# Performance work log

Hardware: AMD Instinct MI355X
Metric: run time of the kernel (lower is better)

Reference implementation:

```python
import jax, jax.numpy as jnp
import numpy as np

B, T, I, H, L = 256, 2000, 80, 20, 2
G = 4 * H  # gates i,f,g,o (PyTorch order)


def _lstm_dir(xg, w_hh, reverse):
    # xg: [B, T, 4H] precomputed input-gate contributions (incl. bias)
    # w_hh: [H, 4H]
    xg_t = jnp.swapaxes(xg, 0, 1)  # [T, B, 4H]
    if reverse:
        xg_t = xg_t[::-1]

    def step(carry, g_x):
        h, c = carry
        gates = g_x + h @ w_hh  # [B, 4H]
        i, f, g, o = jnp.split(gates, 4, axis=-1)
        c = jax.nn.sigmoid(f) * c + jax.nn.sigmoid(i) * jnp.tanh(g)
        h = jax.nn.sigmoid(o) * jnp.tanh(c)
        return (h, c), h

    h0 = jnp.zeros((xg.shape[0], H), xg.dtype)
    _, hs = jax.lax.scan(step, (h0, h0), xg_t)  # hs: [T, B, H]
    if reverse:
        hs = hs[::-1]
    return jnp.swapaxes(hs, 0, 1)  # [B, T, H]


def _bilstm_layer(x, w_ih, w_hh, b):
    # x: [B, T, in], w_ih: [2, in, 4H], w_hh: [2, H, 4H], b: [2, 4H]
    out = []
    for d in range(2):
        xg = jnp.einsum('bti,ig->btg', x, w_ih[d]) + b[d]
        out.append(_lstm_dir(xg, w_hh[d], reverse=(d == 1)))
    return jnp.concatenate(out, axis=-1)  # [B, T, 2H]


def setup_inputs() -> dict:
    key = jax.random.key(0)
    ks = jax.random.split(key, 9)
    s = 1.0 / np.sqrt(H)
    u = lambda k, shp: jax.random.uniform(k, shp, jnp.float32, -s, s)
    return {
        'x': jax.random.normal(ks[0], (B, T, I), jnp.float32),
        'w_ih_l0': u(ks[1], (2, I, G)),
        'w_hh_l0': u(ks[2], (2, H, G)),
        'b_l0': u(ks[3], (2, G)),
        'w_ih_l1': u(ks[4], (2, 2 * H, G)),
        'w_hh_l1': u(ks[5], (2, H, G)),
        'b_l1': u(ks[6], (2, G)),
        'fc_w': u(ks[7], (1, 2 * H)),
        'fc_b': u(ks[8], (1,)),
    }


def reference(x, w_ih_l0, w_hh_l0, b_l0, w_ih_l1, w_hh_l1, b_l1, fc_w, fc_b):
    h = _bilstm_layer(x, w_ih_l0, w_hh_l0, b_l0)      # [B, T, 2H]
    h = _bilstm_layer(h, w_ih_l1, w_hh_l1, b_l1)      # [B, T, 2H]
    out = h @ fc_w.T + fc_b                           # [B, T, 1]
    return out.squeeze(-1)                            # [B, T]
```

## Files before the change

kernel.cpp:

```cpp
#include <hip/hip_runtime.h>
#include <math.h>

#define B_ 256
#define T_ 2000
#define I_ 80
#define H_ 20
#define G_ 80
#define M_ 512000

#define LOG2E 1.442695041f

typedef __attribute__((ext_vector_type(2))) float f32x2;
typedef __attribute__((ext_vector_type(2))) unsigned u32x2;

__device__ __forceinline__ f32x2 mk2(float a, float b) { f32x2 r; r.x = a; r.y = b; return r; }

__device__ __forceinline__ float swap_half(float x, int swapidx) {
#if __has_builtin(__builtin_amdgcn_permlane32_swap)
    u32x2 r = __builtin_amdgcn_permlane32_swap(__float_as_uint(x), __float_as_uint(x), false, false);
    return __uint_as_float(r.y);
#else
    return __uint_as_float((unsigned)__builtin_amdgcn_ds_bpermute(swapidx, (int)__float_as_uint(x)));
#endif
}

#define WS2_STRIDE 332
#define WS2_SIZE   6640

template<int K>
__global__ __launch_bounds__(256) void gemm_xg(
    const float* __restrict__ X,
    const float* __restrict__ Wih,
    const float* __restrict__ Bias,
    float* __restrict__ XG,
    int M)
{
    constexpr int KC = 40;
    __shared__ float ws2[WS2_SIZE];
    __shared__ float xs[KC][100];
    __shared__ float bs[160];

    const int tid  = threadIdx.x;
    const int row0 = blockIdx.x * 96;
    const int tx = tid % 20;
    const int ty = tid / 20;
    const bool run = (ty < 12);

    if (tid < 160) {
        int dd = (tid >= 80);
        int r = tid - 80 * dd;
        int j = r >> 2, g = r & 3;
        float sc = (g == 2) ? 2.0f * LOG2E : -LOG2E;
        bs[tid] = sc * Bias[dd * 80 + g * 20 + j];
    }

    int nrows = M - row0; if (nrows > 96) nrows = 96;

    f32x2 acc[8][4];
    bool first = true;
    const float* wsp = &ws2[tx * WS2_STRIDE];

    for (int kc = 0; kc < K; kc += KC) {
        for (int idx = tid; idx < KC * 160; idx += 256) {
            int i = idx / 160, cc = idx - 160 * i;
            int dd = (cc >= 80), r = cc - 80 * dd;
            int j = r >> 2, g = r & 3;
            float sc = (g == 2) ? 2.0f * LOG2E : -LOG2E;
            ws2[(cc >> 3) * WS2_STRIDE + i * 8 + (cc & 7)] =
                sc * Wih[(dd * K + kc + i) * 80 + g * 20 + j];
        }
        for (int i4 = tid; i4 < (96 * KC) / 4; i4 += 256) {
            int r = i4 / 10;
            int kk = (i4 - 10 * r) * 4;
            float4 v = make_float4(0.f, 0.f, 0.f, 0.f);
            if (r < nrows)
                v = *(const float4*)(X + (long long)(row0 + r) * K + kc + kk);
            xs[kk][r] = v.x; xs[kk + 1][r] = v.y; xs[kk + 2][r] = v.z; xs[kk + 3][r] = v.w;
        }
        __syncthreads();

        if (first) {
            first = false;
            #pragma unroll
            for (int p = 0; p < 4; ++p) {
                const f32x2 bv = mk2(bs[tx * 8 + 2 * p], bs[tx * 8 + 2 * p + 1]);
                #pragma unroll
                for (int r = 0; r < 8; ++r) acc[r][p] = bv;
            }
        }

        if (run) {
            #pragma unroll 4
            for (int k = 0; k < KC; ++k) {
                float a[8];
                f32x2 b2[4];
                *(float4*)&a[0]  = *(const float4*)&xs[k][ty * 8];
                *(float4*)&a[4]  = *(const float4*)&xs[k][ty * 8 + 4];
                *(float4*)&b2[0] = *(const float4*)&wsp[k * 8];
                *(float4*)&b2[2] = *(const float4*)&wsp[k * 8 + 4];
                #pragma unroll
                for (int r = 0; r < 8; ++r) {
                    const f32x2 av = mk2(a[r], a[r]);
                    #pragma unroll
                    for (int p = 0; p < 4; ++p)
                        acc[r][p] = __builtin_elementwise_fma(av, b2[p], acc[r][p]);
                }
            }
        }
        __syncthreads();
    }

    if (run) {
        #pragma unroll
        for (int r = 0; r < 8; ++r) {
            int row = row0 + ty * 8 + r;
            if (row < M) {
                float* dst = XG + (long long)row * 160 + tx * 8;
                *(float4*)(dst)     = *(float4*)&acc[r][0];
                *(float4*)(dst + 4) = *(float4*)&acc[r][2];
            }
        }
    }
}

__global__ __launch_bounds__(256) void gemm_xg_tA(
    const float* __restrict__ H0t,
    const float* __restrict__ Wih,
    const float* __restrict__ Bias,
    float* __restrict__ XG,
    int T)
{
    constexpr int K = 40;
    __shared__ float ws2[WS2_SIZE];
    __shared__ float xs[K][100];
    __shared__ float bs[160];

    const int tid = threadIdx.x;
    const int bb  = blockIdx.x / 21;
    const int tc  = blockIdx.x % 21;
    const int t0  = tc * 96;
    const int tx  = tid % 20;
    const int ty  = tid / 20;
    const bool run = (ty < 12);

    if (tid < 160) {
        int dd = (tid >= 80);
        int r = tid - 80 * dd;
        int j = r >> 2, g = r & 3;
        float sc = (g == 2) ? 2.0f * LOG2E : -LOG2E;
        bs[tid] = sc * Bias[dd * 80 + g * 20 + j];
    }

    int nrows = T - t0; if (nrows > 96) nrows = 96;

    for (int idx = tid; idx < K * 160; idx += 256) {
        int i = idx / 160, cc = idx - 160 * i;
        int dd = (cc >= 80), r = cc - 80 * dd;
        int j = r >> 2, g = r & 3;
        float sc = (g == 2) ? 2.0f * LOG2E : -LOG2E;
        ws2[(cc >> 3) * WS2_STRIDE + i * 8 + (cc & 7)] =
            sc * Wih[(dd * K + i) * 80 + g * 20 + j];
    }
    for (int i4 = tid; i4 < K * 24; i4 += 256) {
        int k = i4 / 24;
        int r = (i4 - 24 * k) * 4;
        float4 v = make_float4(0.f, 0.f, 0.f, 0.f);
        if (r < nrows)
            v = *(const float4*)(H0t + ((long long)bb * 40 + k) * T + t0 + r);
        *(float4*)&xs[k][r] = v;
    }
    __syncthreads();

    f32x2 acc[8][4];
    #pragma unroll
    for (int p = 0; p < 4; ++p) {
        const f32x2 bv = mk2(bs[tx * 8 + 2 * p], bs[tx * 8 + 2 * p + 1]);
        #pragma unroll
        for (int r = 0; r < 8; ++r) acc[r][p] = bv;
    }

    if (run) {
        const float* wsp = &ws2[tx * WS2_STRIDE];
        #pragma unroll 4
        for (int k = 0; k < K; ++k) {
            float a[8];
            f32x2 b2[4];
            *(float4*)&a[0]  = *(const float4*)&xs[k][ty * 8];
            *(float4*)&a[4]  = *(const float4*)&xs[k][ty * 8 + 4];
            *(float4*)&b2[0] = *(const float4*)&wsp[k * 8];
            *(float4*)&b2[2] = *(const float4*)&wsp[k * 8 + 4];
            #pragma unroll
            for (int r = 0; r < 8; ++r) {
                const f32x2 av = mk2(a[r], a[r]);
                #pragma unroll
                for (int p = 0; p < 4; ++p)
                    acc[r][p] = __builtin_elementwise_fma(av, b2[p], acc[r][p]);
            }
        }

        #pragma unroll
        for (int r = 0; r < 8; ++r) {
            int rr = ty * 8 + r;
            if (rr < nrows) {
                long long row = (long long)bb * T + t0 + rr;
                float* dst = XG + row * 160 + tx * 8;
                *(float4*)(dst)     = *(float4*)&acc[r][0];
                *(float4*)(dst + 4) = *(float4*)&acc[r][2];
            }
        }
    }
}

__attribute__((amdgpu_waves_per_eu(1, 1)))
__global__ __launch_bounds__(64) void lstm_scan(
    const float* __restrict__ xg,
    const float* __restrict__ w_hh,
    float* __restrict__ h_out,
    int T)
{
    const int bd   = blockIdx.x;
    const int b    = bd >> 1;
    const int d    = bd & 1;
    const int lane = threadIdx.x & 63;
    const int half = lane >> 5;
    const int j    = lane & 31;
    const bool act_lane = (lane < H_);
    const int jj   = (j < H_) ? j : 0;
    const bool isB = (d == 1);

    const int swapidx = ((lane + 32) & 63) << 2;

    const int gA = half ? 2 : 0;
    const int gB = gA + 1;
    const float scA = half ? (2.0f * LOG2E) : (-LOG2E);
    const float scB = -LOG2E;

    f32x2 wA[10], wB[10];
    const float* wb = w_hh + d * (H_ * G_);
    #pragma unroll
    for (int i = 0; i < 10; ++i) {
        wA[i] = mk2(scA * wb[(2 * i) * G_ + gA * 20 + jj],
                    scA * wb[(2 * i + 1) * G_ + gA * 20 + jj]);
        wB[i] = mk2(scB * wb[(2 * i) * G_ + gB * 20 + jj],
                    scB * wb[(2 * i + 1) * G_ + gB * 20 + jj]);
    }

    float sh[20];
    #pragma unroll
    for (int k = 0; k < 20; ++k) sh[k] = 0.f;
    float c = 0.f;

    const int t0    = isB ? (T - 1) : 0;
    const int rstep = isB ? -160 : 160;
    const float* pf = xg + ((long long)(b * T + t0) * 2 + d) * 80 + 4 * jj + 2 * half;

    float* hp = h_out + ((long long)b * 40 + d * 20 + jj) * T + (isB ? T - 4 : 0);
    const int hgstep = isB ? -4 : 4;

    constexpr int PF = 8;
    f32x2 px[PF];
    #pragma unroll
    for (int s = 0; s < PF; ++s) { px[s] = *(const f32x2*)pf; pf += rstep; }

    float hq0 = 0.f, hq1 = 0.f, hq2 = 0.f, hq3 = 0.f;

    for (int tb = 0; tb < T; tb += PF) {
        #pragma unroll
        for (int s = 0; s < PF; ++s) {
            const f32x2 v = px[s];
            px[s] = *(const f32x2*)pf; pf += rstep;

            f32x2 aA1 = mk2(v.x, 0.f);
            f32x2 aA2 = mk2(0.f, 0.f);
            f32x2 aB1 = mk2(v.y, 0.f);
            f32x2 aB2 = mk2(0.f, 0.f);
            #pragma unroll
            for (int i = 0; i < 5; ++i) {
                const f32x2 hlo = mk2(sh[2 * i],      sh[2 * i + 1]);
                const f32x2 hhi = mk2(sh[10 + 2 * i], sh[11 + 2 * i]);
                aA1 = __builtin_elementwise_fma(wA[i],     hlo, aA1);
                aA2 = __builtin_elementwise_fma(wA[i + 5], hhi, aA2);
                aB1 = __builtin_elementwise_fma(wB[i],     hlo, aB1);
                aB2 = __builtin_elementwise_fma(wB[i + 5], hhi, aB2);
            }
            const f32x2 tA = aA1 + aA2;
            const f32x2 tB = aB1 + aB2;
            const float mA = tA.x + tA.y;
            const float mB = tB.x + tB.y;

            const float sA = __builtin_amdgcn_rcpf(1.0f + __builtin_amdgcn_exp2f(mA));
            const float sB = __builtin_amdgcn_rcpf(1.0f + __builtin_amdgcn_exp2f(mB));

            const float sAx = swap_half(sA, swapidx);
            const float gox = swap_half(sB, swapidx);

            const float gg = fmaf(-2.0f, sAx, 1.0f);
            c = fmaf(sB, c, sA * gg);
            const float th = fmaf(-2.0f,
                __builtin_amdgcn_rcpf(1.0f + __builtin_amdgcn_exp2f(2.0f * LOG2E * c)), 1.0f);
            const float hj = gox * th;

            {
                const int p = s & 3;
                if (p == 0) hq0 = hj;
                else if (p == 1) hq1 = hj;
                else if (p == 2) hq2 = hj;
                else {
                    hq3 = hj;
                    float4 sv;
                    sv.x = isB ? hq3 : hq0;
                    sv.y = isB ? hq2 : hq1;
                    sv.z = isB ? hq1 : hq2;
                    sv.w = isB ? hq0 : hq3;
                    if (act_lane) *(float4*)hp = sv;
                    hp += hgstep;
                }
            }

            #pragma unroll
            for (int k = 0; k < 20; ++k)
                sh[k] = __uint_as_float(__builtin_amdgcn_readlane(__float_as_uint(hj), k));
        }
    }
}

__global__ __launch_bounds__(256) void fc_t(
    const float* __restrict__ H1t,
    const float* __restrict__ Wf,
    const float* __restrict__ Bf,
    float* __restrict__ Out,
    int T)
{
    const int b   = blockIdx.x;
    const int t   = blockIdx.y * 1024 + threadIdx.x * 4;
    if (t > T - 4) return;

    const float bias = Bf[0];
    float4 acc = make_float4(bias, bias, bias, bias);
    const float* base = H1t + (long long)b * 40 * T + t;
    #pragma unroll 8
    for (int u = 0; u < 40; ++u) {
        const float wv = Wf[u];
        const float4 hv = *(const float4*)(base + (long long)u * T);
        acc.x = fmaf(hv.x, wv, acc.x);
        acc.y = fmaf(hv.y, wv, acc.y);
        acc.z = fmaf(hv.z, wv, acc.z);
        acc.w = fmaf(hv.w, wv, acc.w);
    }
    *(float4*)(Out + (long long)b * T + t) = acc;
}

extern "C" void kernel_launch(void* const* d_in, const int* in_sizes, int n_in,
                              void* d_out, int out_size, void* d_ws, size_t ws_size,
                              hipStream_t stream) {
    const float* x     = (const float*)d_in[0];
    const float* wih0  = (const float*)d_in[1];
    const float* whh0  = (const float*)d_in[2];
    const float* b0    = (const float*)d_in[3];
    const float* wih1  = (const float*)d_in[4];
    const float* whh1  = (const float*)d_in[5];
    const float* b1    = (const float*)d_in[6];
    const float* fcw   = (const float*)d_in[7];
    const float* fcb   = (const float*)d_in[8];
    float* out = (float*)d_out;

    float* ws = (float*)d_ws;
    float* xg  = ws + 2048;
    float* h0t = xg + 81920000LL + 2048;
    float* h1t = h0t + 20480000LL;

    const int M = M_;
    const int gemm_grid = (M + 95) / 96;

    gemm_xg<80><<<dim3(gemm_grid), dim3(256), 0, stream>>>(x, wih0, b0, xg, M);
    lstm_scan<<<dim3(B_ * 2), dim3(64), 0, stream>>>(xg, whh0, h0t, T_);
    gemm_xg_tA<<<dim3(B_ * 21), dim3(256), 0, stream>>>(h0t, wih1, b1, xg, T_);
    lstm_scan<<<dim3(B_ * 2), dim3(64), 0, stream>>>(xg, whh1, h1t, T_);
    fc_t<<<dim3(B_, 2), dim3(256), 0, stream>>>(h1t, fcw, fcb, out, T_);
}
```

Measured before the change: 1.334 ms.

## Fuse layer-0 scan with layer-1 input GEMM and layer-1 scan with FC

Combines each per-batch LSTM scan with the following stage in one kernel. One 512-thread block per batch element runs both scan directions in two waves, while the other waves stage the layer-1 weights. After a block barrier the block computes the layer-1 input projection, or the final FC, for that batch element. This removes two kernel launches and lets the downstream work read h0/h1 while it is still in L2 after the scan. The cost is that 384 threads sit idle for the whole sequential scan, and scan occupancy changes from 512 one-wave blocks to 256 eight-wave blocks.

```diff
diff --git a/kernel.cpp b/kernel.cpp
--- a/kernel.cpp
+++ b/kernel.cpp
@@ -123,105 +123,12 @@
     }
 }
 
-__global__ __launch_bounds__(256) void gemm_xg_tA(
-    const float* __restrict__ H0t,
-    const float* __restrict__ Wih,
-    const float* __restrict__ Bias,
-    float* __restrict__ XG,
-    int T)
-{
-    constexpr int K = 40;
-    __shared__ float ws2[WS2_SIZE];
-    __shared__ float xs[K][100];
-    __shared__ float bs[160];
-
-    const int tid = threadIdx.x;
-    const int bb  = blockIdx.x / 21;
-    const int tc  = blockIdx.x % 21;
-    const int t0  = tc * 96;
-    const int tx  = tid % 20;
-    const int ty  = tid / 20;
-    const bool run = (ty < 12);
-
-    if (tid < 160) {
-        int dd = (tid >= 80);
-        int r = tid - 80 * dd;
-        int j = r >> 2, g = r & 3;
-        float sc = (g == 2) ? 2.0f * LOG2E : -LOG2E;
-        bs[tid] = sc * Bias[dd * 80 + g * 20 + j];
-    }
-
-    int nrows = T - t0; if (nrows > 96) nrows = 96;
-
-    for (int idx = tid; idx < K * 160; idx += 256) {
-        int i = idx / 160, cc = idx - 160 * i;
-        int dd = (cc >= 80), r = cc - 80 * dd;
-        int j = r >> 2, g = r & 3;
-        float sc = (g == 2) ? 2.0f * LOG2E : -LOG2E;
-        ws2[(cc >> 3) * WS2_STRIDE + i * 8 + (cc & 7)] =
-            sc * Wih[(dd * K + i) * 80 + g * 20 + j];
-    }
-    for (int i4 = tid; i4 < K * 24; i4 += 256) {
-        int k = i4 / 24;
-        int r = (i4 - 24 * k) * 4;
-        float4 v = make_float4(0.f, 0.f, 0.f, 0.f);
-        if (r < nrows)
-            v = *(const float4*)(H0t + ((long long)bb * 40 + k) * T + t0 + r);
-        *(float4*)&xs[k][r] = v;
-    }
-    __syncthreads();
-
-    f32x2 acc[8][4];
-    #pragma unroll
-    for (int p = 0; p < 4; ++p) {
-        const f32x2 bv = mk2(bs[tx * 8 + 2 * p], bs[tx * 8 + 2 * p + 1]);
-        #pragma unroll
-        for (int r = 0; r < 8; ++r) acc[r][p] = bv;
-    }
-
-    if (run) {
-        const float* wsp = &ws2[tx * WS2_STRIDE];
-        #pragma unroll 4
-        for (int k = 0; k < K; ++k) {
-            float a[8];
-            f32x2 b2[4];
-            *(float4*)&a[0]  = *(const float4*)&xs[k][ty * 8];
-            *(float4*)&a[4]  = *(const float4*)&xs[k][ty * 8 + 4];
-            *(float4*)&b2[0] = *(const float4*)&wsp[k * 8];
-            *(float4*)&b2[2] = *(const float4*)&wsp[k * 8 + 4];
-            #pragma unroll
-            for (int r = 0; r < 8; ++r) {
-                const f32x2 av = mk2(a[r], a[r]);
-                #pragma unroll
-                for (int p = 0; p < 4; ++p)
-                    acc[r][p] = __builtin_elementwise_fma(av, b2[p], acc[r][p]);
-            }
-        }
-
-        #pragma unroll
-        for (int r = 0; r < 8; ++r) {
-            int rr = ty * 8 + r;
-            if (rr < nrows) {
-                long long row = (long long)bb * T + t0 + rr;
-                float* dst = XG + row * 160 + tx * 8;
-                *(float4*)(dst)     = *(float4*)&acc[r][0];
-                *(float4*)(dst + 4) = *(float4*)&acc[r][2];
-            }
-        }
-    }
-}
-
-__attribute__((amdgpu_waves_per_eu(1, 1)))
-__global__ __launch_bounds__(64) void lstm_scan(
+__device__ __forceinline__ void scan_dir(
     const float* __restrict__ xg,
     const float* __restrict__ w_hh,
     float* __restrict__ h_out,
-    int T)
+    int T, int b, int d, int lane)
 {
-    const int bd   = blockIdx.x;
-    const int b    = bd >> 1;
-    const int d    = bd & 1;
-    const int lane = threadIdx.x & 63;
     const int half = lane >> 5;
     const int j    = lane & 31;
     const bool act_lane = (lane < H_);
@@ -324,30 +231,132 @@
     }
 }
 
-__global__ __launch_bounds__(256) void fc_t(
-    const float* __restrict__ H1t,
-    const float* __restrict__ Wf,
-    const float* __restrict__ Bf,
-    float* __restrict__ Out,
+__global__ __launch_bounds__(512) void scan0_gemm1(
+    float* __restrict__ xg,
+    const float* __restrict__ whh0,
+    const float* __restrict__ wih1,
+    const float* __restrict__ b1,
+    float* __restrict__ h0t,
+    int T)
+{
+    __shared__ float ws2s[WS2_SIZE];
+    __shared__ float xs[40][100];
+    __shared__ float bs[160];
+
+    const int b   = blockIdx.x;
+    const int tid = threadIdx.x;
+
+    if (tid >= 128) {
+        for (int idx = tid - 128; idx < 40 * 160; idx += 384) {
+            int i = idx / 160, cc = idx - 160 * i;
+            int dd = (cc >= 80), r = cc - 80 * dd;
+            int jc = r >> 2, g = r & 3;
+            float sc = (g == 2) ? 2.0f * LOG2E : -LOG2E;
+            ws2s[(cc >> 3) * WS2_STRIDE + i * 8 + (cc & 7)] =
+                sc * wih1[(dd * 40 + i) * 80 + g * 20 + jc];
+        }
+        if (tid - 128 < 160) {
+            int cidx = tid - 128;
+            int dd = (cidx >= 80);
+            int r = cidx - 80 * dd;
+            int jc = r >> 2, g = r & 3;
+            float sc = (g == 2) ? 2.0f * LOG2E : -LOG2E;
+            bs[cidx] = sc * b1[dd * 80 + g * 20 + jc];
+        }
+    } else {
+        scan_dir(xg, whh0, h0t, T, b, tid >> 6, tid & 63);
+    }
+    __syncthreads();
+
+    const int tx  = tid % 20;
+    const int tyy = tid / 20;
+    const bool run = (tyy < 24);
+    const float* wsp = &ws2s[tx * WS2_STRIDE];
+
+    for (int tc = 0; tc < 21; ++tc) {
+        const int t0 = tc * 96;
+        int nrows = T - t0; if (nrows > 96) nrows = 96;
+
+        for (int i4 = tid; i4 < 40 * 24; i4 += 512) {
+            int k = i4 / 24;
+            int r = (i4 - 24 * k) * 4;
+            float4 v = make_float4(0.f, 0.f, 0.f, 0.f);
+            if (r < nrows)
+                v = *(const float4*)(h0t + ((long long)b * 40 + k) * T + t0 + r);
+            *(float4*)&xs[k][r] = v;
+        }
+        __syncthreads();
+
+        if (run) {
+            f32x2 acc[4][4];
+            #pragma unroll
+            for (int p = 0; p < 4; ++p) {
+                const f32x2 bv = mk2(bs[tx * 8 + 2 * p], bs[tx * 8 + 2 * p + 1]);
+                #pragma unroll
+                for (int r = 0; r < 4; ++r) acc[r][p] = bv;
+            }
+            #pragma unroll 4
+            for (int k = 0; k < 40; ++k) {
+                float a[4];
+                f32x2 b2[4];
+                *(float4*)&a[0]  = *(const float4*)&xs[k][tyy * 4];
+                *(float4*)&b2[0] = *(const float4*)&wsp[k * 8];
+                *(float4*)&b2[2] = *(const float4*)&wsp[k * 8 + 4];
+                #pragma unroll
+                for (int r = 0; r < 4; ++r) {
+                    const f32x2 av = mk2(a[r], a[r]);
+                    #pragma unroll
+                    for (int p = 0; p < 4; ++p)
+                        acc[r][p] = __builtin_elementwise_fma(av, b2[p], acc[r][p]);
+                }
+            }
+            #pragma unroll
+            for (int r = 0; r < 4; ++r) {
+                int rr = tyy * 4 + r;
+                if (rr < nrows) {
+                    long long row = (long long)b * T + t0 + rr;
+                    float* dst = xg + row * 160 + tx * 8;
+                    *(float4*)(dst)     = *(float4*)&acc[r][0];
+                    *(float4*)(dst + 4) = *(float4*)&acc[r][2];
+                }
+            }
+        }
+        __syncthreads();
+    }
+}
+
+__global__ __launch_bounds__(512) void scan1_fc(
+    const float* __restrict__ xg,
+    const float* __restrict__ whh1,
+    const float* __restrict__ fcw,
+    const float* __restrict__ fcb,
+    float* __restrict__ h1t,
+    float* __restrict__ out,
     int T)
 {
     const int b   = blockIdx.x;
-    const int t   = blockIdx.y * 1024 + threadIdx.x * 4;
-    if (t > T - 4) return;
-
-    const float bias = Bf[0];
-    float4 acc = make_float4(bias, bias, bias, bias);
-    const float* base = H1t + (long long)b * 40 * T + t;
-    #pragma unroll 8
-    for (int u = 0; u < 40; ++u) {
-        const float wv = Wf[u];
-        const float4 hv = *(const float4*)(base + (long long)u * T);
-        acc.x = fmaf(hv.x, wv, acc.x);
-        acc.y = fmaf(hv.y, wv, acc.y);
-        acc.z = fmaf(hv.z, wv, acc.z);
-        acc.w = fmaf(hv.w, wv, acc.w);
-    }
-    *(float4*)(Out + (long long)b * T + t) = acc;
+    const int tid = threadIdx.x;
+
+    if (tid < 128)
+        scan_dir(xg, whh1, h1t, T, b, tid >> 6, tid & 63);
+    __syncthreads();
+
+    const int t = tid * 4;
+    if (t <= T - 4) {
+        const float bias = fcb[0];
+        float4 acc = make_float4(bias, bias, bias, bias);
+        const float* base = h1t + (long long)b * 40 * T + t;
+        #pragma unroll 8
+        for (int u = 0; u < 40; ++u) {
+            const float wv = fcw[u];
+            const float4 hv = *(const float4*)(base + (long long)u * T);
+            acc.x = fmaf(hv.x, wv, acc.x);
+            acc.y = fmaf(hv.y, wv, acc.y);
+            acc.z = fmaf(hv.z, wv, acc.z);
+            acc.w = fmaf(hv.w, wv, acc.w);
+        }
+        *(float4*)(out + (long long)b * T + t) = acc;
+    }
 }
 
 extern "C" void kernel_launch(void* const* d_in, const int* in_sizes, int n_in,
@@ -364,7 +373,7 @@
     const float* fcb   = (const float*)d_in[8];
     float* out = (float*)d_out;
 
-    float* ws = (float*)d_ws;
+    float* ws  = (float*)d_ws;
     float* xg  = ws + 2048;
     float* h0t = xg + 81920000LL + 2048;
     float* h1t = h0t + 20480000LL;
@@ -373,8 +382,6 @@
     const int gemm_grid = (M + 95) / 96;
 
     gemm_xg<80><<<dim3(gemm_grid), dim3(256), 0, stream>>>(x, wih0, b0, xg, M);
-    lstm_scan<<<dim3(B_ * 2), dim3(64), 0, stream>>>(xg, whh0, h0t, T_);
-    gemm_xg_tA<<<dim3(B_ * 21), dim3(256), 0, stream>>>(h0t, wih1, b1, xg, T_);
-    lstm_scan<<<dim3(B_ * 2), dim3(64), 0, stream>>>(xg, whh1, h1t, T_);
-    fc_t<<<dim3(B_, 2), dim3(256), 0, stream>>>(h1t, fcw, fcb, out, T_);
-}
+    scan0_gemm1<<<dim3(B_), dim3(512), 0, stream>>>(xg, whh0, wih1, b1, h0t, T_);
+    scan1_fc<<<dim3(B_), dim3(512), 0, stream>>>(xg, whh1, fcw, fcb, h1t, out, T_);
+}
```

Result: slower. 1.371 ms (+2.8%).
